# Kernel optimization log

Hardware: AMD Instinct MI355X
Metric: run time of the kernel (lower is better)

The kernel has to match this reference:

```python
import jax, jax.numpy as jnp
import numpy as np

B = 500000  # batch rows


def setup_inputs() -> dict:
    key = jax.random.key(0)
    k_x, k_v1, k_v2, k_l1, k_l2, k_l3 = jax.random.split(key, 6)
    return {
        "x": jax.random.normal(k_x, (B, 2), dtype=jnp.float32),
        "varphi1": jax.random.normal(k_v1, (300, 3), dtype=jnp.float32) * 0.1,
        "varphi2": jax.random.normal(k_v2, (1, 300), dtype=jnp.float32) * 0.1,
        "l1_diag": jax.random.normal(k_l1, (3,), dtype=jnp.float32),
        "l2_diag": jax.random.normal(k_l2, (300,), dtype=jnp.float32),
        "l3_diag": jax.random.normal(k_l3, (1,), dtype=jnp.float32),
    }


def reference(x, varphi1, varphi2, l1_diag, l2_diag, l3_diag):
    # append bias column of ones: [B, 3]
    xa = jnp.concatenate([x, jnp.ones((x.shape[0], 1), dtype=x.dtype)], axis=1)
    # diag(v) @ M == v[:, None] * M ; M @ diag(v) == M * v[None, :]
    W_21 = varphi1 * l1_diag[None, :] - l2_diag[:, None] * varphi1          # [300, 3]
    W_32 = varphi2 * l2_diag[None, :] - l3_diag[:, None] * varphi2          # [1, 300]
    W_31 = (l3_diag[:, None] * varphi2 - varphi2 * l2_diag[None, :]) @ varphi1  # [1, 3]
    # y = W_31 @ xa^T + W_32 @ relu(W_21 @ xa^T), returned transposed -> [B, 1]
    h = jax.nn.relu(xa @ W_21.T)                                            # [B, 300]
    y = xa @ W_31.T + h @ W_32.T                                            # [B, 1]
    return y
```

## Files before the change

### kernel.cpp

```cpp
#include <hip/hip_runtime.h>

#define NH 300
#define BLK 256
#define RPT 4


__global__ __launch_bounds__(320)
void phi2_precompute(const float* __restrict__ varphi1,
                     const float* __restrict__ varphi2,
                     const float* __restrict__ l1,
                     const float* __restrict__ l2,
                     const float* __restrict__ l3,
                     float4* __restrict__ coef,
                     float* __restrict__ w31p) {
    __shared__ float red[5][3];
    int j = threadIdx.x;
    float p0 = 0.f, p1 = 0.f, p2 = 0.f;
    if (j < NH) {
        float lv2  = l2[j];
        float phi2 = varphi2[j];
        float W32 = phi2 * (lv2 - l3[0]);
        float v0 = varphi1[j*3+0], v1 = varphi1[j*3+1], v2 = varphi1[j*3+2];
        float a = v0 * (l1[0] - lv2);
        float b = v1 * (l1[1] - lv2);
        float c = v2 * (l1[2] - lv2);
        coef[j] = make_float4(a, b, c, 0.5f * W32);
        p0 = W32 * (0.5f * a - v0);
        p1 = W32 * (0.5f * b - v1);
        p2 = W32 * (0.5f * c - v2);
    }
    for (int off = 32; off > 0; off >>= 1) {
        p0 += __shfl_down(p0, off);
        p1 += __shfl_down(p1, off);
        p2 += __shfl_down(p2, off);
    }
    int wave = threadIdx.x >> 6;
    if ((threadIdx.x & 63) == 0) {
        red[wave][0] = p0; red[wave][1] = p1; red[wave][2] = p2;
    }
    __syncthreads();
    if (threadIdx.x == 0) {
        float s0 = 0.f, s1 = 0.f, s2 = 0.f;
        for (int w = 0; w < 5; ++w) { s0 += red[w][0]; s1 += red[w][1]; s2 += red[w][2]; }
        w31p[0] = s0; w31p[1] = s1; w31p[2] = s2;
    }
}

__global__ __launch_bounds__(BLK)
void phi2_main(const float* __restrict__ x,
               const float4* __restrict__ coef,
               const float* __restrict__ w31p,
               float* __restrict__ y,
               int B) {
    __shared__ float4 scoef[NH];
    for (int i = threadIdx.x; i < NH; i += BLK) scoef[i] = coef[i];
    float w0 = w31p[0], w1 = w31p[1], w2 = w31p[2];
    __syncthreads();

    int base = blockIdx.x * (BLK * RPT) + threadIdx.x;
    float x0[RPT], x1[RPT], acc[RPT];
#pragma unroll
    for (int r = 0; r < RPT; ++r) {
        int row = base + r * BLK;
        float2 xv = (row < B) ? ((const float2*)x)[row] : make_float2(0.f, 0.f);
        x0[r] = xv.x; x1[r] = xv.y;
        acc[r] = fmaf(w0, xv.x, fmaf(w1, xv.y, w2));
    }

#pragma unroll 4
    for (int j = 0; j < NH; ++j) {
        float4 cf = scoef[j];
#pragma unroll
        for (int r = 0; r < RPT; ++r) {
            float d = fmaf(cf.x, x0[r], fmaf(cf.y, x1[r], cf.z));
            acc[r] = fmaf(cf.w, fabsf(d), acc[r]);
        }
    }

#pragma unroll
    for (int r = 0; r < RPT; ++r) {
        int row = base + r * BLK;
        if (row < B) y[row] = acc[r];
    }
}

extern "C" void kernel_launch(void* const* d_in, const int* in_sizes, int n_in,
                              void* d_out, int out_size, void* d_ws, size_t ws_size,
                              hipStream_t stream) {
    const float* x       = (const float*)d_in[0];
    const float* varphi1 = (const float*)d_in[1];
    const float* varphi2 = (const float*)d_in[2];
    const float* l1      = (const float*)d_in[3];
    const float* l2      = (const float*)d_in[4];
    const float* l3      = (const float*)d_in[5];

    float4* coef = (float4*)d_ws;
    float*  w31p = (float*)((char*)d_ws + NH * sizeof(float4));
    float*  y    = (float*)d_out;

    int B = in_sizes[0] / 2;

    phi2_precompute<<<1, 320, 0, stream>>>(varphi1, varphi2, l1, l2, l3, coef, w31p);

    int grid = (B + BLK * RPT - 1) / (BLK * RPT);
    phi2_main<<<grid, BLK, 0, stream>>>(x, coef, w31p, y, B);
}
```

Before: 81.44 us.

## Read coefficients from global/scalar cache and vectorize per-thread row loads

Drops the shared-memory staging of the 300 coefficient float4s and the block barrier, reading coef[j] directly from global memory. The loop index is uniform across the wave, so the compiler can fetch these through scalar loads. Each thread now owns four contiguous rows, loading x with two float4 reads and storing y with one float4 write, with an early exit for out-of-range threads. This removes LDS traffic and the sync from the compute-bound inner loop, but per-lane vector accesses are strided across the wave, which may reduce coalescing.

```diff
diff --git a/kernel.cpp b/kernel.cpp
--- a/kernel.cpp
+++ b/kernel.cpp
@@ -52,24 +52,36 @@
                const float* __restrict__ w31p,
                float* __restrict__ y,
                int B) {
-    __shared__ float4 scoef[NH];
-    for (int i = threadIdx.x; i < NH; i += BLK) scoef[i] = coef[i];
+    long t  = (long)blockIdx.x * BLK + threadIdx.x;
+    long r0 = t * RPT;
+    if (r0 >= B) return;
+
     float w0 = w31p[0], w1 = w31p[1], w2 = w31p[2];
-    __syncthreads();
 
-    int base = blockIdx.x * (BLK * RPT) + threadIdx.x;
     float x0[RPT], x1[RPT], acc[RPT];
+    bool full = (r0 + RPT <= B);
+    if (full) {
+        float4 xa = *(const float4*)(x + 2 * r0);
+        float4 xb = *(const float4*)(x + 2 * r0 + 4);
+        x0[0] = xa.x; x1[0] = xa.y;
+        x0[1] = xa.z; x1[1] = xa.w;
+        x0[2] = xb.x; x1[2] = xb.y;
+        x0[3] = xb.z; x1[3] = xb.w;
+    } else {
 #pragma unroll
-    for (int r = 0; r < RPT; ++r) {
-        int row = base + r * BLK;
-        float2 xv = (row < B) ? ((const float2*)x)[row] : make_float2(0.f, 0.f);
-        x0[r] = xv.x; x1[r] = xv.y;
-        acc[r] = fmaf(w0, xv.x, fmaf(w1, xv.y, w2));
+        for (int r = 0; r < RPT; ++r) {
+            long row = r0 + r;
+            if (row < B) { x0[r] = x[2*row]; x1[r] = x[2*row+1]; }
+            else         { x0[r] = 0.f;      x1[r] = 0.f; }
+        }
     }
+#pragma unroll
+    for (int r = 0; r < RPT; ++r)
+        acc[r] = fmaf(w0, x0[r], fmaf(w1, x1[r], w2));
 
 #pragma unroll 4
     for (int j = 0; j < NH; ++j) {
-        float4 cf = scoef[j];
+        const float4 cf = coef[j];
 #pragma unroll
         for (int r = 0; r < RPT; ++r) {
             float d = fmaf(cf.x, x0[r], fmaf(cf.y, x1[r], cf.z));
@@ -77,10 +89,12 @@
         }
     }
 
+    if (full) {
+        *(float4*)(y + r0) = make_float4(acc[0], acc[1], acc[2], acc[3]);
+    } else {
 #pragma unroll
-    for (int r = 0; r < RPT; ++r) {
-        int row = base + r * BLK;
-        if (row < B) y[row] = acc[r];
+        for (int r = 0; r < RPT; ++r)
+            if (r0 + r < B) y[r0 + r] = acc[r];
     }
 }
 
@@ -102,6 +116,7 @@
 
     phi2_precompute<<<1, 320, 0, stream>>>(varphi1, varphi2, l1, l2, l3, coef, w31p);
 
-    int grid = (B + BLK * RPT - 1) / (BLK * RPT);
+    int threads = (B + RPT - 1) / RPT;
+    int grid = (threads + BLK - 1) / BLK;
     phi2_main<<<grid, BLK, 0, stream>>>(x, coef, w31p, y, B);
 }
```

Result: slower. 93.72 us (+15.1%).

## Broadcast hidden-unit coefficients via readlane and process eight contiguous rows per thread

Applied to the files above, without the earlier changes.

Removes the shared-memory coefficient table. Each wavefront now holds 64 coefficients per lane register and broadcasts them with readlane, so the inner loop takes its operands from scalar registers instead of LDS reads. The precompute divides each hidden unit's b and c by a and folds |a| into the output weight. Each thread handles 8 contiguous rows, loading x with float4 loads and storing y with float4 stores. The normalization clamps tiny a, which slightly changes the arithmetic, and the tail handling assumes B is divisible by 8.

```diff
diff --git a/kernel.cpp b/kernel.cpp
--- a/kernel.cpp
+++ b/kernel.cpp
@@ -1,11 +1,12 @@
 #include <hip/hip_runtime.h>
 
-#define NH 300
-#define BLK 256
-#define RPT 4
+#define NH   300
+#define NPAD 320
+#define BLK  256
+#define RPT  8
 
 
-__global__ __launch_bounds__(320)
+__global__ __launch_bounds__(NPAD)
 void phi2_precompute(const float* __restrict__ varphi1,
                      const float* __restrict__ varphi2,
                      const float* __restrict__ l1,
@@ -13,21 +14,25 @@
                      const float* __restrict__ l3,
                      float4* __restrict__ coef,
                      float* __restrict__ w31p) {
-    __shared__ float red[5][3];
+    __shared__ float red[NPAD/64][3];
     int j = threadIdx.x;
     float p0 = 0.f, p1 = 0.f, p2 = 0.f;
     if (j < NH) {
         float lv2  = l2[j];
         float phi2 = varphi2[j];
-        float W32 = phi2 * (lv2 - l3[0]);
+        float W32  = phi2 * (lv2 - l3[0]);
+        float s    = 0.5f * W32;
         float v0 = varphi1[j*3+0], v1 = varphi1[j*3+1], v2 = varphi1[j*3+2];
         float a = v0 * (l1[0] - lv2);
         float b = v1 * (l1[1] - lv2);
         float c = v2 * (l1[2] - lv2);
-        coef[j] = make_float4(a, b, c, 0.5f * W32);
+        float asafe = (fabsf(a) > 1e-20f) ? a : copysignf(1e-20f, a);
+        coef[j] = make_float4(b / asafe, c / asafe, s * fabsf(asafe), 0.f);
         p0 = W32 * (0.5f * a - v0);
         p1 = W32 * (0.5f * b - v1);
         p2 = W32 * (0.5f * c - v2);
+    } else {
+        coef[j] = make_float4(0.f, 0.f, 0.f, 0.f);
     }
     for (int off = 32; off > 0; off >>= 1) {
         p0 += __shfl_down(p0, off);
@@ -41,9 +46,13 @@
     __syncthreads();
     if (threadIdx.x == 0) {
         float s0 = 0.f, s1 = 0.f, s2 = 0.f;
-        for (int w = 0; w < 5; ++w) { s0 += red[w][0]; s1 += red[w][1]; s2 += red[w][2]; }
+        for (int w = 0; w < NPAD/64; ++w) { s0 += red[w][0]; s1 += red[w][1]; s2 += red[w][2]; }
         w31p[0] = s0; w31p[1] = s1; w31p[2] = s2;
     }
+}
+
+__device__ __forceinline__ float rl(float v, int lane) {
+    return __uint_as_float(__builtin_amdgcn_readlane(__float_as_uint(v), lane));
 }
 
 __global__ __launch_bounds__(BLK)
@@ -51,36 +60,56 @@
                const float4* __restrict__ coef,
                const float* __restrict__ w31p,
                float* __restrict__ y,
-               int B) {
-    __shared__ float4 scoef[NH];
-    for (int i = threadIdx.x; i < NH; i += BLK) scoef[i] = coef[i];
+               int nthreads) {
+    int t    = blockIdx.x * BLK + threadIdx.x;
+    int lane = threadIdx.x & 63;
+    bool active = (t < nthreads);
+    int tc = active ? t : (nthreads - 1);
+
+    const float4* xq = (const float4*)x + (size_t)tc * 4;
+    float4 xa = xq[0], xb = xq[1], xc = xq[2], xd = xq[3];
+    float X0[RPT] = {xa.x, xa.z, xb.x, xb.z, xc.x, xc.z, xd.x, xd.z};
+    float X1[RPT] = {xa.y, xa.w, xb.y, xb.w, xc.y, xc.w, xd.y, xd.w};
+
     float w0 = w31p[0], w1 = w31p[1], w2 = w31p[2];
-    __syncthreads();
+    float acc[RPT];
+#pragma unroll
+    for (int r = 0; r < RPT; ++r)
+        acc[r] = fmaf(w0, X0[r], fmaf(w1, X1[r], w2));
 
-    int base = blockIdx.x * (BLK * RPT) + threadIdx.x;
-    float x0[RPT], x1[RPT], acc[RPT];
+    float4 cur = coef[lane];
 #pragma unroll
-    for (int r = 0; r < RPT; ++r) {
-        int row = base + r * BLK;
-        float2 xv = (row < B) ? ((const float2*)x)[row] : make_float2(0.f, 0.f);
-        x0[r] = xv.x; x1[r] = xv.y;
-        acc[r] = fmaf(w0, xv.x, fmaf(w1, xv.y, w2));
+    for (int ch = 0; ch < 4; ++ch) {
+        float4 nxt = coef[(ch + 1) * 64 + lane];
+#pragma unroll 4
+        for (int jj = 0; jj < 64; ++jj) {
+            float Bv = rl(cur.x, jj);
+            float Cv = rl(cur.y, jj);
+            float Av = rl(cur.z, jj);
+#pragma unroll
+            for (int r = 0; r < RPT; ++r) {
+                float tt = fmaf(Bv, X1[r], X0[r]) + Cv;
+                acc[r] = fmaf(Av, fabsf(tt), acc[r]);
+            }
+        }
+        cur = nxt;
     }
-
 #pragma unroll 4
-    for (int j = 0; j < NH; ++j) {
-        float4 cf = scoef[j];
+    for (int jj = 0; jj < 44; ++jj) {
+        float Bv = rl(cur.x, jj);
+        float Cv = rl(cur.y, jj);
+        float Av = rl(cur.z, jj);
 #pragma unroll
         for (int r = 0; r < RPT; ++r) {
-            float d = fmaf(cf.x, x0[r], fmaf(cf.y, x1[r], cf.z));
-            acc[r] = fmaf(cf.w, fabsf(d), acc[r]);
+            float tt = fmaf(Bv, X1[r], X0[r]) + Cv;
+            acc[r] = fmaf(Av, fabsf(tt), acc[r]);
         }
     }
 
-#pragma unroll
-    for (int r = 0; r < RPT; ++r) {
-        int row = base + r * BLK;
-        if (row < B) y[row] = acc[r];
+    if (active) {
+        float4* yq = (float4*)y + (size_t)t * 2;
+        yq[0] = make_float4(acc[0], acc[1], acc[2], acc[3]);
+        yq[1] = make_float4(acc[4], acc[5], acc[6], acc[7]);
     }
 }
 
@@ -95,13 +124,14 @@
     const float* l3      = (const float*)d_in[5];
 
     float4* coef = (float4*)d_ws;
-    float*  w31p = (float*)((char*)d_ws + NH * sizeof(float4));
+    float*  w31p = (float*)((char*)d_ws + NPAD * sizeof(float4));
     float*  y    = (float*)d_out;
 
     int B = in_sizes[0] / 2;
 
-    phi2_precompute<<<1, 320, 0, stream>>>(varphi1, varphi2, l1, l2, l3, coef, w31p);
+    phi2_precompute<<<1, NPAD, 0, stream>>>(varphi1, varphi2, l1, l2, l3, coef, w31p);
 
-    int grid = (B + BLK * RPT - 1) / (BLK * RPT);
-    phi2_main<<<grid, BLK, 0, stream>>>(x, coef, w31p, y, B);
+    int nthreads = (B + RPT - 1) / RPT;
+    int grid = (nthreads + BLK - 1) / BLK;
+    phi2_main<<<grid, BLK, 0, stream>>>(x, coef, w31p, y, nthreads);
 }
```

Measured after the change: 83.92 us. 3.0% more time.
